# Kernel tuning notes

Measured on AMD Instinct MI355X. Metric: run time of the kernel, lower is better.

The kernel has to match this reference:

```python
import jax, jax.numpy as jnp
import numpy as np

B, T, D, H, E, TOP_K = 2, 2048, 1024, 4096, 8, 2


def setup_inputs() -> dict:
    key = jax.random.key(0)
    ks = jax.random.split(key, 7)
    s_d = 1.0 / np.sqrt(D)
    s_h = 1.0 / np.sqrt(H)
    return {
        "x": jax.random.normal(ks[0], (B, T, D), dtype=jnp.float32),
        "gate_w": jax.random.uniform(ks[1], (D, E), minval=-s_d, maxval=s_d, dtype=jnp.float32),
        "gate_b": jax.random.uniform(ks[2], (E,), minval=-s_d, maxval=s_d, dtype=jnp.float32),
        "w1": jax.random.uniform(ks[3], (E, D, H), minval=-s_d, maxval=s_d, dtype=jnp.float32),
        "b1": jax.random.uniform(ks[4], (E, H), minval=-s_d, maxval=s_d, dtype=jnp.float32),
        "w2": jax.random.uniform(ks[5], (E, H, D), minval=-s_h, maxval=s_h, dtype=jnp.float32),
        "b2": jax.random.uniform(ks[6], (E, D), minval=-s_h, maxval=s_h, dtype=jnp.float32),
    }


def reference(x, gate_w, gate_b, w1, b1, w2, b2):
    Bsz, Tn, Din = x.shape
    x_flat = x.reshape(-1, Din)                       # [N, D]
    N = x_flat.shape[0]
    gating_logits = x_flat @ gate_w + gate_b          # [N, E]
    weights, indices = jax.lax.top_k(gating_logits, TOP_K)
    weights = jax.nn.softmax(weights, axis=-1).astype(x.dtype)
    # scatter top-k weights into dense dispatch tensor [N, E]
    dispatch = jnp.zeros((N, E), dtype=x.dtype).at[jnp.arange(N)[:, None], indices].set(weights)
    # NOTE: faithful to original - gate weight multiplies the expert INPUT
    # and again the expert OUTPUT (double weighting through the GELU MLP).
    dispatched_x = dispatch[:, :, None] * x_flat[:, None, :]       # [N, E, D]
    h = jax.nn.gelu(jnp.einsum('ned,edh->neh', dispatched_x, w1) + b1, approximate=False)
    expert_out = jnp.einsum('neh,ehd->ned', h, w2) + b2            # [N, E, D]
    combined = jnp.sum(dispatch[:, :, None] * expert_out, axis=1)  # [N, D]
    final = combined.reshape(Bsz, Tn, -1)
    return final, gating_logits
```

## Files before the change

### kernel.cpp

```cpp
#include <hip/hip_runtime.h>
#include <hip/hip_bf16.h>
#include <math.h>

#define NTOK 4096
#define DDIM 1024
#define HDIM 4096
#define NEXP 8
#define CAP  4096
#define ROWCAP 9216

typedef __attribute__((ext_vector_type(8))) short short8;
typedef __attribute__((ext_vector_type(4))) float f32x4;

#define GLOAD_LDS16(g, l) __builtin_amdgcn_global_load_lds( \
    (const __attribute__((address_space(1))) void*)(g),     \
    (__attribute__((address_space(3))) void*)(l), 16, 0, 0)

__global__ __launch_bounds__(256) void zero_kernel(float* __restrict__ outF,
                                                   int* __restrict__ counts) {
  int i = blockIdx.x * 256 + threadIdx.x;
  float4 z = make_float4(0.f, 0.f, 0.f, 0.f);
  ((float4*)outF)[i] = z;
  if (blockIdx.x == 0 && threadIdx.x < NEXP) counts[threadIdx.x] = 0;
}

__global__ __launch_bounds__(256) void gating_kernel(
    const float* __restrict__ x, const float* __restrict__ gw,
    const float* __restrict__ gb, float* __restrict__ logits_out,
    int* __restrict__ counts, int* __restrict__ tok, float* __restrict__ gate) {
  int t = blockIdx.x;
  int tid = threadIdx.x;
  float p[NEXP];
#pragma unroll
  for (int e = 0; e < NEXP; ++e) p[e] = 0.f;
  const float* xr = x + (size_t)t * DDIM;
  for (int d = tid; d < DDIM; d += 256) {
    float xv = xr[d];
    const float* wr = gw + (size_t)d * NEXP;
#pragma unroll
    for (int e = 0; e < NEXP; ++e) p[e] += xv * wr[e];
  }
#pragma unroll
  for (int off = 32; off > 0; off >>= 1)
#pragma unroll
    for (int e = 0; e < NEXP; ++e) p[e] += __shfl_xor(p[e], off, 64);
  __shared__ float red[4][NEXP];
  int wave = tid >> 6, lane = tid & 63;
  if (lane == 0)
#pragma unroll
    for (int e = 0; e < NEXP; ++e) red[wave][e] = p[e];
  __syncthreads();
  if (tid < NEXP) {
    float v = red[0][tid] + red[1][tid] + red[2][tid] + red[3][tid] + gb[tid];
    logits_out[(size_t)t * NEXP + tid] = v;
    red[0][tid] = v;
  }
  __syncthreads();
  if (tid == 0) {
    float v[NEXP];
#pragma unroll
    for (int e = 0; e < NEXP; ++e) v[e] = red[0][e];
    int i0 = 0;
#pragma unroll
    for (int e = 1; e < NEXP; ++e) if (v[e] > v[i0]) i0 = e;
    int i1 = (i0 == 0) ? 1 : 0;
#pragma unroll
    for (int e = 0; e < NEXP; ++e) if (e != i0 && v[e] > v[i1]) i1 = e;
    float e1 = expf(v[i1] - v[i0]);
    float s = 1.f + e1;
    float g0 = 1.f / s, g1 = e1 / s;
    int s0 = atomicAdd(&counts[i0], 1);
    tok[i0 * CAP + s0] = t; gate[i0 * CAP + s0] = g0;
    int s1 = atomicAdd(&counts[i1], 1);
    tok[i1 * CAP + s1] = t; gate[i1 * CAP + s1] = g1;
  }
}

__global__ void sched_kernel(const int* __restrict__ counts, int* __restrict__ poff) {
  if (threadIdx.x == 0) {
    int acc = 0;
    for (int e = 0; e < NEXP; ++e) {
      poff[e] = acc;
      acc += ((counts[e] + 127) >> 7) << 7;
    }
    poff[NEXP] = acc;
  }
}

__global__ __launch_bounds__(256) void transpose_kernel(
    const float* __restrict__ in, __hip_bfloat16* __restrict__ out, int R, int C) {
  __shared__ float tile[32][33];
  int e = blockIdx.z;
  int c0 = blockIdx.x * 32, r0 = blockIdx.y * 32;
  int tx = threadIdx.x & 31, ty = threadIdx.x >> 5;
  const float* inp = in + (size_t)e * R * C;
  __hip_bfloat16* outp = out + (size_t)e * R * C;
#pragma unroll
  for (int i = 0; i < 32; i += 8)
    tile[ty + i][tx] = inp[(size_t)(r0 + ty + i) * C + c0 + tx];
  __syncthreads();
#pragma unroll
  for (int i = 0; i < 32; i += 8)
    outp[(size_t)(c0 + ty + i) * R + r0 + tx] = __float2bfloat16(tile[tx][ty + i]);
}

__global__ __launch_bounds__(256) void gather_kernel(
    const float* __restrict__ x, const int* __restrict__ counts,
    const int* __restrict__ poff, const int* __restrict__ tok,
    const float* __restrict__ gate, __hip_bfloat16* __restrict__ Xg) {
  int e = blockIdx.y, r = blockIdx.x;
  int pc = poff[e + 1] - poff[e];
  if (r >= pc) return;
  int row = poff[e] + r;
  int tid = threadIdx.x;
  __hip_bfloat16* orow = Xg + (size_t)row * DDIM;
  if (r < counts[e]) {
    int t = tok[e * CAP + r];
    float g = gate[e * CAP + r];
    float4 v = ((const float4*)(x + (size_t)t * DDIM))[tid];
    union { unsigned short u[4]; uint2 q; } pk;
    __hip_bfloat16 h0 = __float2bfloat16(v.x * g);
    __hip_bfloat16 h1 = __float2bfloat16(v.y * g);
    __hip_bfloat16 h2 = __float2bfloat16(v.z * g);
    __hip_bfloat16 h3 = __float2bfloat16(v.w * g);
    pk.u[0] = *(unsigned short*)&h0; pk.u[1] = *(unsigned short*)&h1;
    pk.u[2] = *(unsigned short*)&h2; pk.u[3] = *(unsigned short*)&h3;
    ((uint2*)orow)[tid] = pk.q;
  } else {
    uint2 z; z.x = 0; z.y = 0;
    ((uint2*)orow)[tid] = z;
  }
}

template <int EPI>
__global__ __launch_bounds__(256) void moe_gemm(
    const __hip_bfloat16* __restrict__ A, const __hip_bfloat16* __restrict__ B,
    const float* __restrict__ bias, __hip_bfloat16* __restrict__ Hout,
    float* __restrict__ Out, const int* __restrict__ counts,
    const int* __restrict__ poff, const int* __restrict__ tok,
    const float* __restrict__ gate, int K, int Nn) {
  int e = blockIdx.z;
  int rt = blockIdx.y;
  int p0 = poff[e], p1 = poff[e + 1];
  int pcount = p1 - p0;
  if (rt * 128 >= pcount) return;
  int rowBase = p0 + rt * 128;
  int colBase = blockIdx.x * 128;

  __shared__ __align__(16) char As[128 * 64];
  __shared__ __align__(16) char Bs[128 * 64];

  const char* Ae = (const char*)A + (size_t)rowBase * K * 2;
  const char* Be = (const char*)B + ((size_t)e * Nn + colBase) * (size_t)K * 2;

  int tid = threadIdx.x;
  int wave = tid >> 6, lane = tid & 63;
  int srow = lane >> 2;
  int sbyte = (lane & 3) * 16;

  f32x4 acc[4][4] = {};

  int wm = (wave >> 1) * 64, wn = (wave & 1) * 64;
  int frm = lane & 15;
  int fko = (lane >> 4) * 16;

  for (int k0 = 0; k0 < K; k0 += 32) {
    __syncthreads();
#pragma unroll
    for (int c = 0; c < 2; ++c) {
      int ch = wave * 2 + c;
      int r = ch * 16 + srow;
      GLOAD_LDS16(Ae + ((size_t)r * K + k0) * 2 + sbyte, As + ch * 1024 + lane * 16);
      GLOAD_LDS16(Be + ((size_t)r * K + k0) * 2 + sbyte, Bs + ch * 1024 + lane * 16);
    }
    __syncthreads();
    short8 af[4], bf[4];
#pragma unroll
    for (int i = 0; i < 4; ++i) {
      af[i] = *(const short8*)(As + (wm + i * 16 + frm) * 64 + fko);
      bf[i] = *(const short8*)(Bs + (wn + i * 16 + frm) * 64 + fko);
    }
#pragma unroll
    for (int i = 0; i < 4; ++i)
#pragma unroll
      for (int j = 0; j < 4; ++j)
        acc[i][j] = __builtin_amdgcn_mfma_f32_16x16x32_bf16(af[i], bf[j], acc[i][j], 0, 0, 0);
  }

  int cq = lane >> 4, cn = lane & 15;
  if (EPI == 0) {
#pragma unroll
    for (int i = 0; i < 4; ++i) {
#pragma unroll
      for (int j = 0; j < 4; ++j) {
        int col = colBase + wn + j * 16 + cn;
        float bv = bias[e * Nn + col];
#pragma unroll
        for (int r = 0; r < 4; ++r) {
          int row = rowBase + wm + i * 16 + cq * 4 + r;
          float v = acc[i][j][r] + bv;
          v = 0.5f * v * (1.0f + erff(v * 0.70710678118f));
          Hout[(size_t)row * Nn + col] = __float2bfloat16(v);
        }
      }
    }
  } else {
    int cnt = counts[e];
#pragma unroll
    for (int i = 0; i < 4; ++i) {
#pragma unroll
      for (int r = 0; r < 4; ++r) {
        int rloc = rt * 128 + wm + i * 16 + cq * 4 + r;
        if (rloc < cnt) {
          int t = tok[e * CAP + rloc];
          float g = gate[e * CAP + rloc];
#pragma unroll
          for (int j = 0; j < 4; ++j) {
            int col = colBase + wn + j * 16 + cn;
            float v = g * (acc[i][j][r] + bias[e * Nn + col]);
            atomicAdd(Out + (size_t)t * DDIM + col, v);
          }
        }
      }
    }
  }
}

extern "C" void kernel_launch(void* const* d_in, const int* in_sizes, int n_in,
                              void* d_out, int out_size, void* d_ws, size_t ws_size,
                              hipStream_t stream) {
  const float* x  = (const float*)d_in[0];
  const float* gw = (const float*)d_in[1];
  const float* gb = (const float*)d_in[2];
  const float* w1 = (const float*)d_in[3];
  const float* b1 = (const float*)d_in[4];
  const float* w2 = (const float*)d_in[5];
  const float* b2 = (const float*)d_in[6];

  float* outF = (float*)d_out;
  float* outL = outF + (size_t)NTOK * DDIM;

  size_t off = 0;
  char* base = (char*)d_ws;
  auto alloc = [&](size_t bytes) {
    void* r = base + off;
    off += (bytes + 255) & ~(size_t)255;
    return r;
  };
  __hip_bfloat16* wT1 = (__hip_bfloat16*)alloc((size_t)NEXP * HDIM * DDIM * 2);
  __hip_bfloat16* wT2 = (__hip_bfloat16*)alloc((size_t)NEXP * DDIM * HDIM * 2);
  __hip_bfloat16* Xg  = (__hip_bfloat16*)alloc((size_t)ROWCAP * DDIM * 2);
  __hip_bfloat16* Hact= (__hip_bfloat16*)alloc((size_t)ROWCAP * HDIM * 2);
  int*   tok    = (int*)alloc((size_t)NEXP * CAP * 4);
  float* gate   = (float*)alloc((size_t)NEXP * CAP * 4);
  int*   counts = (int*)alloc(64);
  int*   poff   = (int*)alloc(64);

  zero_kernel<<<(NTOK * DDIM) / (256 * 4), 256, 0, stream>>>(outF, counts);
  gating_kernel<<<NTOK, 256, 0, stream>>>(x, gw, gb, outL, counts, tok, gate);
  sched_kernel<<<1, 64, 0, stream>>>(counts, poff);
  transpose_kernel<<<dim3(HDIM / 32, DDIM / 32, NEXP), 256, 0, stream>>>(w1, wT1, DDIM, HDIM);
  transpose_kernel<<<dim3(DDIM / 32, HDIM / 32, NEXP), 256, 0, stream>>>(w2, wT2, HDIM, DDIM);
  gather_kernel<<<dim3(CAP, NEXP), 256, 0, stream>>>(x, counts, poff, tok, gate, Xg);
  moe_gemm<0><<<dim3(HDIM / 128, 32, NEXP), 256, 0, stream>>>(
      Xg, wT1, b1, Hact, nullptr, counts, poff, tok, gate, DDIM, HDIM);
  moe_gemm<1><<<dim3(DDIM / 128, 32, NEXP), 256, 0, stream>>>(
      Hact, wT2, b2, nullptr, outF, counts, poff, tok, gate, HDIM, DDIM);
}
```

Before: 735.9 us.

## Compact MoE tile schedule, split-K second GEMM, swizzled LDS, deterministic combine

```diff
diff --git a/kernel.cpp b/kernel.cpp
--- a/kernel.cpp
+++ b/kernel.cpp
@@ -8,6 +8,7 @@
 #define NEXP 8
 #define CAP  4096
 #define ROWCAP 9216
+#define MAXTILES 72
 
 typedef __attribute__((ext_vector_type(8))) short short8;
 typedef __attribute__((ext_vector_type(4))) float f32x4;
@@ -16,18 +17,11 @@
     (const __attribute__((address_space(1))) void*)(g),     \
     (__attribute__((address_space(3))) void*)(l), 16, 0, 0)
 
-__global__ __launch_bounds__(256) void zero_kernel(float* __restrict__ outF,
-                                                   int* __restrict__ counts) {
-  int i = blockIdx.x * 256 + threadIdx.x;
-  float4 z = make_float4(0.f, 0.f, 0.f, 0.f);
-  ((float4*)outF)[i] = z;
-  if (blockIdx.x == 0 && threadIdx.x < NEXP) counts[threadIdx.x] = 0;
-}
-
 __global__ __launch_bounds__(256) void gating_kernel(
     const float* __restrict__ x, const float* __restrict__ gw,
     const float* __restrict__ gb, float* __restrict__ logits_out,
-    int* __restrict__ counts, int* __restrict__ tok, float* __restrict__ gate) {
+    int* __restrict__ counts, int* __restrict__ tok, float* __restrict__ gate,
+    int* __restrict__ eA, int* __restrict__ sA, float* __restrict__ gA) {
   int t = blockIdx.x;
   int tid = threadIdx.x;
   float p[NEXP];
@@ -73,35 +67,55 @@
     tok[i0 * CAP + s0] = t; gate[i0 * CAP + s0] = g0;
     int s1 = atomicAdd(&counts[i1], 1);
     tok[i1 * CAP + s1] = t; gate[i1 * CAP + s1] = g1;
-  }
-}
-
-__global__ void sched_kernel(const int* __restrict__ counts, int* __restrict__ poff) {
+    eA[2 * t] = i0; sA[2 * t] = s0; gA[2 * t] = g0;
+    eA[2 * t + 1] = i1; sA[2 * t + 1] = s1; gA[2 * t + 1] = g1;
+  }
+}
+
+__global__ void sched_kernel(const int* __restrict__ counts, int* __restrict__ poff,
+                             int* __restrict__ tileE, int* __restrict__ tileR,
+                             int* __restrict__ nTiles) {
   if (threadIdx.x == 0) {
-    int acc = 0;
+    int acc = 0, nt = 0;
     for (int e = 0; e < NEXP; ++e) {
       poff[e] = acc;
-      acc += ((counts[e] + 127) >> 7) << 7;
+      int tl = (counts[e] + 127) >> 7;
+      for (int t = 0; t < tl; ++t) { tileE[nt] = e; tileR[nt] = acc + t * 128; ++nt; }
+      acc += tl << 7;
     }
     poff[NEXP] = acc;
+    nTiles[0] = nt;
   }
 }
 
 __global__ __launch_bounds__(256) void transpose_kernel(
     const float* __restrict__ in, __hip_bfloat16* __restrict__ out, int R, int C) {
-  __shared__ float tile[32][33];
+  __shared__ float tile[64 * 65];
   int e = blockIdx.z;
-  int c0 = blockIdx.x * 32, r0 = blockIdx.y * 32;
-  int tx = threadIdx.x & 31, ty = threadIdx.x >> 5;
+  int c0 = blockIdx.x * 64, r0 = blockIdx.y * 64;
   const float* inp = in + (size_t)e * R * C;
   __hip_bfloat16* outp = out + (size_t)e * R * C;
-#pragma unroll
-  for (int i = 0; i < 32; i += 8)
-    tile[ty + i][tx] = inp[(size_t)(r0 + ty + i) * C + c0 + tx];
+  int tx = threadIdx.x & 15, ty = threadIdx.x >> 4;
+#pragma unroll
+  for (int i = 0; i < 64; i += 16) {
+    float4 v = *(const float4*)(inp + (size_t)(r0 + ty + i) * C + c0 + tx * 4);
+    float* dst = tile + (ty + i) * 65 + tx * 4;
+    dst[0] = v.x; dst[1] = v.y; dst[2] = v.z; dst[3] = v.w;
+  }
   __syncthreads();
-#pragma unroll
-  for (int i = 0; i < 32; i += 8)
-    outp[(size_t)(c0 + ty + i) * R + r0 + tx] = __float2bfloat16(tile[tx][ty + i]);
+  int c = threadIdx.x >> 3;
+  int rb = (threadIdx.x & 7) * 8;
+#pragma unroll
+  for (int p = 0; p < 2; ++p) {
+    int cc = c + p * 32;
+    union { unsigned short u[8]; short8 v8; } pk;
+#pragma unroll
+    for (int j = 0; j < 8; ++j) {
+      __hip_bfloat16 h = __float2bfloat16(tile[(rb + j) * 65 + cc]);
+      pk.u[j] = *(unsigned short*)&h;
+    }
+    *(short8*)(outp + (size_t)(c0 + cc) * R + r0 + rb) = pk.v8;
+  }
 }
 
 __global__ __launch_bounds__(256) void gather_kernel(
@@ -136,15 +150,13 @@
 __global__ __launch_bounds__(256) void moe_gemm(
     const __hip_bfloat16* __restrict__ A, const __hip_bfloat16* __restrict__ B,
     const float* __restrict__ bias, __hip_bfloat16* __restrict__ Hout,
-    float* __restrict__ Out, const int* __restrict__ counts,
-    const int* __restrict__ poff, const int* __restrict__ tok,
-    const float* __restrict__ gate, int K, int Nn) {
-  int e = blockIdx.z;
-  int rt = blockIdx.y;
-  int p0 = poff[e], p1 = poff[e + 1];
-  int pcount = p1 - p0;
-  if (rt * 128 >= pcount) return;
-  int rowBase = p0 + rt * 128;
+    float* __restrict__ Pout, const int* __restrict__ tileE,
+    const int* __restrict__ tileR, const int* __restrict__ nTiles,
+    int K, int Nn) {
+  int ty = blockIdx.y;
+  if (ty >= nTiles[0]) return;
+  int e = tileE[ty];
+  int rowBase = tileR[ty];
   int colBase = blockIdx.x * 128;
 
   __shared__ __align__(16) char As[128 * 64];
@@ -156,35 +168,38 @@
   int tid = threadIdx.x;
   int wave = tid >> 6, lane = tid & 63;
   int srow = lane >> 2;
-  int sbyte = (lane & 3) * 16;
+  int cg = (((lane & 3) ^ ((lane >> 3) & 3)) << 4);
 
   f32x4 acc[4][4] = {};
 
   int wm = (wave >> 1) * 64, wn = (wave & 1) * 64;
   int frm = lane & 15;
-  int fko = (lane >> 4) * 16;
-
-  for (int k0 = 0; k0 < K; k0 += 32) {
+  int fsw = (((lane >> 4) ^ ((lane >> 1) & 3)) << 4);
+
+  int kPer = (EPI == 1) ? (K >> 1) : K;
+  int kLo = blockIdx.z * kPer, kHi = kLo + kPer;
+
+  for (int k0 = kLo; k0 < kHi; k0 += 32) {
     __syncthreads();
 #pragma unroll
     for (int c = 0; c < 2; ++c) {
       int ch = wave * 2 + c;
       int r = ch * 16 + srow;
-      GLOAD_LDS16(Ae + ((size_t)r * K + k0) * 2 + sbyte, As + ch * 1024 + lane * 16);
-      GLOAD_LDS16(Be + ((size_t)r * K + k0) * 2 + sbyte, Bs + ch * 1024 + lane * 16);
+      GLOAD_LDS16(Ae + ((size_t)r * K + k0) * 2 + cg, As + ch * 1024 + lane * 16);
+      GLOAD_LDS16(Be + ((size_t)r * K + k0) * 2 + cg, Bs + ch * 1024 + lane * 16);
     }
     __syncthreads();
-    short8 af[4], bf[4];
+    short8 af[4], bfr[4];
 #pragma unroll
     for (int i = 0; i < 4; ++i) {
-      af[i] = *(const short8*)(As + (wm + i * 16 + frm) * 64 + fko);
-      bf[i] = *(const short8*)(Bs + (wn + i * 16 + frm) * 64 + fko);
+      af[i]  = *(const short8*)(As + (wm + i * 16 + frm) * 64 + fsw);
+      bfr[i] = *(const short8*)(Bs + (wn + i * 16 + frm) * 64 + fsw);
     }
 #pragma unroll
     for (int i = 0; i < 4; ++i)
 #pragma unroll
       for (int j = 0; j < 4; ++j)
-        acc[i][j] = __builtin_amdgcn_mfma_f32_16x16x32_bf16(af[i], bf[j], acc[i][j], 0, 0, 0);
+        acc[i][j] = __builtin_amdgcn_mfma_f32_16x16x32_bf16(af[i], bfr[j], acc[i][j], 0, 0, 0);
   }
 
   int cq = lane >> 4, cn = lane & 15;
@@ -205,25 +220,43 @@
       }
     }
   } else {
-    int cnt = counts[e];
+    float* Pp = Pout + ((size_t)blockIdx.z * ROWCAP + rowBase) * DDIM;
 #pragma unroll
     for (int i = 0; i < 4; ++i) {
 #pragma unroll
-      for (int r = 0; r < 4; ++r) {
-        int rloc = rt * 128 + wm + i * 16 + cq * 4 + r;
-        if (rloc < cnt) {
-          int t = tok[e * CAP + rloc];
-          float g = gate[e * CAP + rloc];
-#pragma unroll
-          for (int j = 0; j < 4; ++j) {
-            int col = colBase + wn + j * 16 + cn;
-            float v = g * (acc[i][j][r] + bias[e * Nn + col]);
-            atomicAdd(Out + (size_t)t * DDIM + col, v);
-          }
+      for (int j = 0; j < 4; ++j) {
+        int col = colBase + wn + j * 16 + cn;
+#pragma unroll
+        for (int r = 0; r < 4; ++r) {
+          int row = wm + i * 16 + cq * 4 + r;
+          Pp[(size_t)row * DDIM + col] = acc[i][j][r];
         }
       }
     }
   }
+}
+
+__global__ __launch_bounds__(256) void combine_kernel(
+    const float* __restrict__ P, const float* __restrict__ b2,
+    const int* __restrict__ poff, const int* __restrict__ eA,
+    const int* __restrict__ sA, const float* __restrict__ gA,
+    float* __restrict__ outF) {
+  int t = blockIdx.x, c = threadIdx.x;
+  int e0 = eA[2 * t], e1 = eA[2 * t + 1];
+  int r0 = poff[e0] + sA[2 * t], r1 = poff[e1] + sA[2 * t + 1];
+  float g0 = gA[2 * t], g1 = gA[2 * t + 1];
+  float4 a0 = ((const float4*)(P + (size_t)r0 * DDIM))[c];
+  float4 a1 = ((const float4*)(P + ((size_t)ROWCAP + r0) * DDIM))[c];
+  float4 b0 = ((const float4*)(P + (size_t)r1 * DDIM))[c];
+  float4 b1 = ((const float4*)(P + ((size_t)ROWCAP + r1) * DDIM))[c];
+  float4 bb0 = ((const float4*)(b2 + (size_t)e0 * DDIM))[c];
+  float4 bb1 = ((const float4*)(b2 + (size_t)e1 * DDIM))[c];
+  float4 o;
+  o.x = g0 * (a0.x + a1.x + bb0.x) + g1 * (b0.x + b1.x + bb1.x);
+  o.y = g0 * (a0.y + a1.y + bb0.y) + g1 * (b0.y + b1.y + bb1.y);
+  o.z = g0 * (a0.z + a1.z + bb0.z) + g1 * (b0.z + b1.z + bb1.z);
+  o.w = g0 * (a0.w + a1.w + bb0.w) + g1 * (b0.w + b1.w + bb1.w);
+  ((float4*)(outF + (size_t)t * DDIM))[c] = o;
 }
 
 extern "C" void kernel_launch(void* const* d_in, const int* in_sizes, int n_in,
@@ -248,22 +281,30 @@
     return r;
   };
   __hip_bfloat16* wT1 = (__hip_bfloat16*)alloc((size_t)NEXP * HDIM * DDIM * 2);
+  __hip_bfloat16* Xg  = (__hip_bfloat16*)alloc((size_t)ROWCAP * DDIM * 2);
   __hip_bfloat16* wT2 = (__hip_bfloat16*)alloc((size_t)NEXP * DDIM * HDIM * 2);
-  __hip_bfloat16* Xg  = (__hip_bfloat16*)alloc((size_t)ROWCAP * DDIM * 2);
   __hip_bfloat16* Hact= (__hip_bfloat16*)alloc((size_t)ROWCAP * HDIM * 2);
   int*   tok    = (int*)alloc((size_t)NEXP * CAP * 4);
   float* gate   = (float*)alloc((size_t)NEXP * CAP * 4);
+  int*   eA     = (int*)alloc((size_t)NTOK * 2 * 4);
+  int*   sA     = (int*)alloc((size_t)NTOK * 2 * 4);
+  float* gA     = (float*)alloc((size_t)NTOK * 2 * 4);
   int*   counts = (int*)alloc(64);
   int*   poff   = (int*)alloc(64);
-
-  zero_kernel<<<(NTOK * DDIM) / (256 * 4), 256, 0, stream>>>(outF, counts);
-  gating_kernel<<<NTOK, 256, 0, stream>>>(x, gw, gb, outL, counts, tok, gate);
-  sched_kernel<<<1, 64, 0, stream>>>(counts, poff);
-  transpose_kernel<<<dim3(HDIM / 32, DDIM / 32, NEXP), 256, 0, stream>>>(w1, wT1, DDIM, HDIM);
-  transpose_kernel<<<dim3(DDIM / 32, HDIM / 32, NEXP), 256, 0, stream>>>(w2, wT2, HDIM, DDIM);
+  int*   tileE  = (int*)alloc(MAXTILES * 4);
+  int*   tileR  = (int*)alloc(MAXTILES * 4);
+  int*   nTiles = (int*)alloc(64);
+  float* P      = (float*)wT1;
+
+  hipMemsetAsync(counts, 0, 64, stream);
+  gating_kernel<<<NTOK, 256, 0, stream>>>(x, gw, gb, outL, counts, tok, gate, eA, sA, gA);
+  sched_kernel<<<1, 64, 0, stream>>>(counts, poff, tileE, tileR, nTiles);
+  transpose_kernel<<<dim3(HDIM / 64, DDIM / 64, NEXP), 256, 0, stream>>>(w1, wT1, DDIM, HDIM);
+  transpose_kernel<<<dim3(DDIM / 64, HDIM / 64, NEXP), 256, 0, stream>>>(w2, wT2, HDIM, DDIM);
   gather_kernel<<<dim3(CAP, NEXP), 256, 0, stream>>>(x, counts, poff, tok, gate, Xg);
-  moe_gemm<0><<<dim3(HDIM / 128, 32, NEXP), 256, 0, stream>>>(
-      Xg, wT1, b1, Hact, nullptr, counts, poff, tok, gate, DDIM, HDIM);
-  moe_gemm<1><<<dim3(DDIM / 128, 32, NEXP), 256, 0, stream>>>(
-      Hact, wT2, b2, nullptr, outF, counts, poff, tok, gate, HDIM, DDIM);
-}
+  moe_gemm<0><<<dim3(HDIM / 128, MAXTILES, 1), 256, 0, stream>>>(
+      Xg, wT1, b1, Hact, nullptr, tileE, tileR, nTiles, DDIM, HDIM);
+  moe_gemm<1><<<dim3(DDIM / 128, MAXTILES, 2), 256, 0, stream>>>(
+      Hact, wT2, b2, nullptr, P, tileE, tileR, nTiles, HDIM, DDIM);
+  combine_kernel<<<NTOK, 256, 0, stream>>>(P, b2, poff, eA, sA, gA, outF);
+}
```

Result: faster. 720.4 us (-2.1%).
